# Kernel tuning notes

Measured on AMD Instinct MI355X. Metric: run time of the kernel, lower is better.

## Reference

```python
import jax, jax.numpy as jnp
import numpy as np

C = 1024
RANK = 8


def _layernorm(x, g, b, eps=1e-5):
    mu = jnp.mean(x, axis=-1, keepdims=True)
    var = jnp.var(x, axis=-1, keepdims=True)
    return (x - mu) * jax.lax.rsqrt(var + eps) * g + b


def setup_inputs() -> dict:
    key = jax.random.key(0)
    ks = jax.random.split(key, 10)
    B, T = 4, 4096
    x = jax.random.normal(ks[0], (B, T, C), dtype=jnp.float32)
    # parameters (match torch inits)
    W0 = jnp.eye(C, dtype=jnp.float32) * 0.1
    A_init = jax.random.normal(ks[1], (C, RANK), dtype=jnp.float32) * 0.01
    B_init = jnp.zeros((RANK, C), dtype=jnp.float32)
    log_lr = jnp.full((C,), float(np.log(0.1)), dtype=jnp.float32)
    s = 1.0 / np.sqrt(C)
    Wq = jax.random.uniform(ks[2], (C, C), minval=-s, maxval=s, dtype=jnp.float32)
    Wk = jax.random.uniform(ks[3], (C, C), minval=-s, maxval=s, dtype=jnp.float32)
    Wv = jax.random.uniform(ks[4], (C, C), minval=-s, maxval=s, dtype=jnp.float32)
    Wo = jax.random.uniform(ks[5], (C, C), minval=-s, maxval=s, dtype=jnp.float32)
    Wg = jax.random.uniform(ks[6], (C, C), minval=-s, maxval=s, dtype=jnp.float32)
    ln_g = jnp.ones((C,), dtype=jnp.float32)
    ln_b = jnp.zeros((C,), dtype=jnp.float32)
    ls_g = jnp.full((C,), 1e-4, dtype=jnp.float32)  # LayerScale gamma
    return {"x": x, "W0": W0, "A_init": A_init, "B_init": B_init,
            "log_lr": log_lr, "Wq": Wq, "Wk": Wk, "Wv": Wv, "Wo": Wo,
            "Wg": Wg, "ln_g": ln_g, "ln_b": ln_b, "ls_g": ls_g}


def reference(x, W0, A_init, B_init, log_lr, Wq, Wk, Wv, Wo, Wg, ln_g, ln_b, ls_g):
    B, T, _ = x.shape
    h = _layernorm(x, ln_g, ln_b)
    # dual-form TTT (training path: q/k/v projections, full K @ W0)
    Q = jnp.einsum('btc,dc->btd', h, Wq)
    K = jnp.einsum('btc,dc->btd', h, Wk)
    V = jnp.einsum('btc,dc->btd', h, Wv)
    lr = jnp.minimum(jnp.exp(log_lr), 1.0)  # clamp(max=1.0)
    y0 = jnp.einsum('btc,cd->btd', K, W0) + jnp.einsum('btr,rd->btd', jnp.einsum('btc,cr->btr', K, A_init), B_init)
    error = y0 - V
    loss = jnp.mean(error ** 2)
    gradient = K * error                     # [B,T,C]
    grad_cumsum = jnp.cumsum(gradient, axis=1)
    grad_shift = jnp.concatenate([jnp.zeros((B, 1, gradient.shape[-1]), gradient.dtype), grad_cumsum[:, :-1, :]], axis=1)
    correction = Q * lr[None, None, :] * grad_shift
    pos = jnp.arange(1, T + 1, dtype=correction.dtype)
    pos_scale = (1.0 / (1.0 + 0.1 * jnp.log(pos)))[None, :, None]
    out = y0 - correction * pos_scale
    # gate, out projection, layer scale, residual
    gate = jax.nn.sigmoid(jnp.einsum('btc,dc->btd', x, Wg))
    out = out * gate
    out = jnp.einsum('btc,dc->btd', out, Wo) * ls_g
    return (x + out, loss)
```

## Files before the change

### kernel.cpp

```cpp
#include <hip/hip_runtime.h>
#include <stdint.h>
#include <math.h>

typedef unsigned short u16;
typedef __attribute__((ext_vector_type(8))) short short8;
typedef __attribute__((ext_vector_type(4))) float f32x4;

__device__ __forceinline__ float bf2f(u16 u){
  union { unsigned int i; float f; } v; v.i = ((unsigned int)u) << 16; return v.f;
}
__device__ __forceinline__ u16 f2bf(float f){
  union { float f; unsigned int i; } v; v.f = f;
  return (u16)((v.i + 0x7FFFu + ((v.i >> 16) & 1u)) >> 16);
}

__global__ void ln_prep(const float* __restrict__ x, const float* __restrict__ g,
                        const float* __restrict__ bta, u16* __restrict__ h,
                        u16* __restrict__ xb, float* __restrict__ loss){
  if (blockIdx.x == 0 && threadIdx.x == 0) loss[0] = 0.f;
  int row = blockIdx.x, tid = threadIdx.x;
  const float4* xr = (const float4*)(x + (size_t)row * 1024);
  float4 v = xr[tid];
  float s  = v.x + v.y + v.z + v.w;
  float s2 = v.x*v.x + v.y*v.y + v.z*v.z + v.w*v.w;
  #pragma unroll
  for (int o = 32; o > 0; o >>= 1){ s += __shfl_down(s, o); s2 += __shfl_down(s2, o); }
  __shared__ float red[8];
  if ((tid & 63) == 0){ red[tid >> 6] = s; red[4 + (tid >> 6)] = s2; }
  __syncthreads();
  float ts = red[0]+red[1]+red[2]+red[3];
  float t2 = red[4]+red[5]+red[6]+red[7];
  float mu   = ts * (1.0f/1024.0f);
  float var  = t2 * (1.0f/1024.0f) - mu*mu;
  float rstd = rsqrtf(var + 1e-5f);
  float4 gg = ((const float4*)g)[tid];
  float4 bb = ((const float4*)bta)[tid];
  ushort4 hv, xv;
  hv.x = f2bf((v.x-mu)*rstd*gg.x + bb.x);
  hv.y = f2bf((v.y-mu)*rstd*gg.y + bb.y);
  hv.z = f2bf((v.z-mu)*rstd*gg.z + bb.z);
  hv.w = f2bf((v.w-mu)*rstd*gg.w + bb.w);
  xv.x = f2bf(v.x); xv.y = f2bf(v.y); xv.z = f2bf(v.z); xv.w = f2bf(v.w);
  ((ushort4*)h )[(size_t)row*256 + tid] = hv;
  ((ushort4*)xb)[(size_t)row*256 + tid] = xv;
}

__global__ void conv5(const float* __restrict__ a, const float* __restrict__ b,
                      const float* __restrict__ c, const float* __restrict__ d,
                      const float* __restrict__ e,
                      u16* oa, u16* ob, u16* oc, u16* od, u16* oe){
  int sel = blockIdx.y;
  const float* s = sel==0?a : sel==1?b : sel==2?c : sel==3?d : e;
  u16* o = sel==0?oa : sel==1?ob : sel==2?oc : sel==3?od : oe;
  int i = blockIdx.x*256 + threadIdx.x;
  float4 v = ((const float4*)s)[i];
  ushort4 r; r.x=f2bf(v.x); r.y=f2bf(v.y); r.z=f2bf(v.z); r.w=f2bf(v.w);
  ((ushort4*)o)[i] = r;
}

__global__ void weff_k(const float* __restrict__ W0, const float* __restrict__ Ai,
                       const float* __restrict__ Bi, u16* __restrict__ Wet){
  __shared__ float tile[32][33];
  int d0 = blockIdx.x*32, e0 = blockIdx.y*32;
  int tid = threadIdx.x;
  int lr = tid >> 5, lc = tid & 31;
  #pragma unroll
  for (int s = 0; s < 4; ++s){
    int e = e0 + s*8 + lr, d = d0 + lc;
    float v = W0[(size_t)e*1024 + d];
    #pragma unroll
    for (int r = 0; r < 8; ++r) v += Ai[e*8 + r] * Bi[(size_t)r*1024 + d];
    tile[s*8 + lr][lc] = v;
  }
  __syncthreads();
  #pragma unroll
  for (int s = 0; s < 4; ++s){
    int d = d0 + s*8 + lr, e = e0 + lc;
    Wet[(size_t)d*1024 + e] = f2bf(tile[lc][s*8 + lr]);
  }
}

#define VMW(N)  asm volatile("s_waitcnt vmcnt(" #N ")" ::: "memory")
#define SBAR    __builtin_amdgcn_s_barrier()
#define SCHED0  __builtin_amdgcn_sched_barrier(0)

template<int EPI>
__device__ __forceinline__ void gemm256_body(const u16* __restrict__ A, const u16* __restrict__ Bm,
    u16* __restrict__ Cb, float* __restrict__ Cf, const float* __restrict__ lsg,
    const float* __restrict__ xres, int mblk, int nblk)
{
  __shared__ u16 As[4][8192];
  __shared__ u16 Bs[4][8192];
  const int tid  = threadIdx.x;
  const int lane = tid & 63;
  const int w    = tid >> 6;
  const int wm = w >> 2, wn = w & 3;
  const int l15 = lane & 15, quad = lane >> 4;
  const int m0 = mblk * 256, n0 = nblk * 256;

  const int sl   = (lane & 7) ^ (lane >> 3);
  const int srow = 2*(w*8 + (lane >> 3)) + (sl >> 2);
  const int scol = (sl & 3) * 8;
  const u16* gA = A  + (size_t)(m0 + srow)*1024 + scol;
  const u16* gB = Bm + (size_t)(n0 + srow)*1024 + scol;
  const int ldsOff = w * 512;

  const int phys8 = (((((l15 & 1) << 2) | quad) ^ (l15 >> 1))) * 8;
  const int rdA = (wm*64 + (l15 >> 1))*64 + phys8;
  const int rdB = (wn*32 + (l15 >> 1))*64 + phys8;

  f32x4 acc[8][4] = {};

#define SA(T) do{ const int _ss=(T)&3; const size_t _k=(size_t)(T)*32; \
    __builtin_amdgcn_global_load_lds((const __attribute__((address_space(1))) unsigned int*)(gA + _k), \
        (__attribute__((address_space(3))) unsigned int*)(&As[_ss][ldsOff]), 16, 0, 0); \
    __builtin_amdgcn_global_load_lds((const __attribute__((address_space(1))) unsigned int*)(gA + _k + 131072), \
        (__attribute__((address_space(3))) unsigned int*)(&As[_ss][ldsOff + 4096]), 16, 0, 0); \
  }while(0)
#define SB(T) do{ const int _ss=(T)&3; const size_t _k=(size_t)(T)*32; \
    __builtin_amdgcn_global_load_lds((const __attribute__((address_space(1))) unsigned int*)(gB + _k), \
        (__attribute__((address_space(3))) unsigned int*)(&Bs[_ss][ldsOff]), 16, 0, 0); \
    __builtin_amdgcn_global_load_lds((const __attribute__((address_space(1))) unsigned int*)(gB + _k + 131072), \
        (__attribute__((address_space(3))) unsigned int*)(&Bs[_ss][ldsOff + 4096]), 16, 0, 0); \
  }while(0)

#define SLICE(T, VMOP, DS) do{ \
    VMOP; \
    SCHED0; SBAR; SCHED0; \
    if (DS){ SA((T)+3); SB((T)+3); } \
    const int _s = (T) & 3; \
    const u16* _as = &As[_s][0]; \
    const u16* _bs = &Bs[_s][0]; \
    short8 afv[8], bfv[4]; \
    _Pragma("unroll") \
    for (int _j = 0; _j < 4; ++_j) bfv[_j] = *(const short8*)(_bs + rdB + _j*512); \
    _Pragma("unroll") \
    for (int _i = 0; _i < 8; ++_i) afv[_i] = *(const short8*)(_as + rdA + _i*512); \
    _Pragma("unroll") \
    for (int _i = 0; _i < 8; ++_i){ \
      _Pragma("unroll") \
      for (int _j = 0; _j < 4; ++_j) \
        acc[_i][_j] = __builtin_amdgcn_mfma_f32_16x16x32_bf16(afv[_i], bfv[_j], acc[_i][_j], 0, 0, 0); \
    } \
  }while(0)

  SA(0); SB(0); SA(1); SB(1); SA(2); SB(2);

  #pragma unroll 1
  for (int t = 0; t < 28; t += 4){
    SLICE(t+0, VMW(8), 1);
    SLICE(t+1, VMW(8), 1);
    SLICE(t+2, VMW(8), 1);
    SLICE(t+3, VMW(8), 1);
  }
  SLICE(28, VMW(8), 1);
  SLICE(29, VMW(8), 0);
  SLICE(30, VMW(4), 0);
  SLICE(31, VMW(0), 0);
#undef SLICE
#undef SA
#undef SB

  const int rbase = quad * 4;
  if (EPI == 0){
    #pragma unroll
    for (int i = 0; i < 8; ++i){
      int row = m0 + wm*128 + i*16 + rbase;
      #pragma unroll
      for (int j = 0; j < 4; ++j){
        int col = n0 + wn*64 + j*16 + l15;
        #pragma unroll
        for (int r = 0; r < 4; ++r)
          Cb[(size_t)(row + r)*1024 + col] = f2bf(acc[i][j][r]);
      }
    }
  } else {
    float lsv[4];
    #pragma unroll
    for (int j = 0; j < 4; ++j) lsv[j] = lsg[n0 + wn*64 + j*16 + l15];
    #pragma unroll
    for (int i = 0; i < 8; ++i){
      int row = m0 + wm*128 + i*16 + rbase;
      #pragma unroll
      for (int j = 0; j < 4; ++j){
        int col = n0 + wn*64 + j*16 + l15;
        #pragma unroll
        for (int r = 0; r < 4; ++r){
          size_t idx = (size_t)(row + r)*1024 + col;
          Cf[idx] = acc[i][j][r] * lsv[j] + xres[idx];
        }
      }
    }
  }
}

__global__ __launch_bounds__(512, 2) void gemm_qkvg(
    const u16* __restrict__ h, const u16* __restrict__ xb,
    const u16* __restrict__ Wqb, const u16* __restrict__ Wkb,
    const u16* __restrict__ Wvb, const u16* __restrict__ Wgb,
    u16* __restrict__ Qb, u16* __restrict__ Kb,
    u16* __restrict__ Vb, u16* __restrict__ Gb){
  int bid = blockIdx.x;
  int swz = (bid & 7) * 128 + (bid >> 3);
  int mblk = swz >> 4;
  int rem  = swz & 15;
  int sel  = rem >> 2, nblk = rem & 3;
  const u16* A  = (sel == 3) ? xb : h;
  const u16* Bm = sel==0?Wqb : sel==1?Wkb : sel==2?Wvb : Wgb;
  u16* Out      = sel==0?Qb  : sel==1?Kb  : sel==2?Vb  : Gb;
  gemm256_body<0>(A, Bm, Out, nullptr, nullptr, nullptr, mblk, nblk);
}

__global__ __launch_bounds__(512, 2) void gemm_plain(
    const u16* __restrict__ A, const u16* __restrict__ Bm, u16* __restrict__ C){
  int bid = blockIdx.x;
  int swz = (bid & 7) * 32 + (bid >> 3);
  gemm256_body<0>(A, Bm, C, nullptr, nullptr, nullptr, swz >> 2, swz & 3);
}

__global__ __launch_bounds__(512, 2) void gemm_final(
    const u16* __restrict__ A, const u16* __restrict__ Bm,
    float* __restrict__ C, const float* __restrict__ lsg,
    const float* __restrict__ xres){
  int bid = blockIdx.x;
  int swz = (bid & 7) * 32 + (bid >> 3);
  gemm256_body<1>(A, Bm, nullptr, C, lsg, xres, swz >> 2, swz & 3);
}

__global__ void scan1(const u16* __restrict__ Kb, const u16* __restrict__ Vb,
                      const u16* __restrict__ Yb, float* __restrict__ part,
                      float* __restrict__ loss){
  int tid = threadIdx.x;
  int c = blockIdx.x*256 + tid;
  int ch = blockIdx.y, b = blockIdx.z;
  size_t base = ((size_t)b*4096 + (size_t)ch*128)*1024 + c;
  float g = 0.f, ls = 0.f;
  #pragma unroll 8
  for (int t = 0; t < 128; ++t){
    size_t idx = base + (size_t)t*1024;
    float kv = bf2f(Kb[idx]), vv = bf2f(Vb[idx]), yv = bf2f(Yb[idx]);
    float e = yv - vv;
    g += kv*e; ls += e*e;
  }
  part[((size_t)(b*32 + ch))*1024 + c] = g;
  #pragma unroll
  for (int o = 32; o > 0; o >>= 1) ls += __shfl_down(ls, o);
  __shared__ float red[4];
  if ((tid & 63) == 0) red[tid >> 6] = ls;
  __syncthreads();
  if (tid == 0) atomicAdd(loss, red[0]+red[1]+red[2]+red[3]);
}

__global__ void scan2(const u16* __restrict__ Kb, const u16* __restrict__ Vb,
                      const u16* __restrict__ Yb, const u16* __restrict__ Qb,
                      const u16* __restrict__ Gb, const float* __restrict__ part,
                      const float* __restrict__ llr, u16* __restrict__ OutPre){
  int tid = threadIdx.x;
  int c = blockIdx.x*256 + tid;
  int ch = blockIdx.y, b = blockIdx.z;
  float run = 0.f;
  for (int j = 0; j < ch; ++j) run += part[((size_t)(b*32 + j))*1024 + c];
  float lrc = fminf(expf(llr[c]), 1.0f);
  size_t base = ((size_t)b*4096 + (size_t)ch*128)*1024 + c;
  #pragma unroll 4
  for (int t = 0; t < 128; ++t){
    size_t idx = base + (size_t)t*1024;
    float kv = bf2f(Kb[idx]), vv = bf2f(Vb[idx]), yv = bf2f(Yb[idx]);
    float qv = bf2f(Qb[idx]), gl = bf2f(Gb[idx]);
    float e = yv - vv;
    int tg = ch*128 + t + 1;
    float ps = 1.0f/(1.0f + 0.1f*logf((float)tg));
    float gate = 1.0f/(1.0f + expf(-gl));
    float o = (yv - qv*lrc*run*ps) * gate;
    OutPre[idx] = f2bf(o);
    run += kv*e;
  }
}

__global__ void finloss(const float* __restrict__ loss, float* __restrict__ o){
  o[0] = loss[0] * (1.0f/16777216.0f);
}

extern "C" void kernel_launch(void* const* d_in, const int* in_sizes, int n_in,
                              void* d_out, int out_size, void* d_ws, size_t ws_size,
                              hipStream_t stream){
  const float* x   = (const float*)d_in[0];
  const float* W0  = (const float*)d_in[1];
  const float* Ai  = (const float*)d_in[2];
  const float* Bi  = (const float*)d_in[3];
  const float* llr = (const float*)d_in[4];
  const float* Wq  = (const float*)d_in[5];
  const float* Wk  = (const float*)d_in[6];
  const float* Wv  = (const float*)d_in[7];
  const float* Wo  = (const float*)d_in[8];
  const float* Wg  = (const float*)d_in[9];
  const float* lng = (const float*)d_in[10];
  const float* lnb = (const float*)d_in[11];
  const float* lsg = (const float*)d_in[12];
  float* out = (float*)d_out;

  const size_t TOK = 16384, CC = 1024;
  char* p = (char*)d_ws;
  float* loss = (float*)p; p += 256;
  u16* h   = (u16*)p; p += TOK*CC*2;
  u16* xb  = (u16*)p; p += TOK*CC*2;
  u16* Qb  = (u16*)p; p += TOK*CC*2;
  u16* Kb  = (u16*)p; p += TOK*CC*2;
  u16* Vb  = (u16*)p; p += TOK*CC*2;
  u16* Gb  = (u16*)p; p += TOK*CC*2;
  u16* Wqb = (u16*)p; p += CC*CC*2;
  u16* Wkb = (u16*)p; p += CC*CC*2;
  u16* Wvb = (u16*)p; p += CC*CC*2;
  u16* Wgb = (u16*)p; p += CC*CC*2;
  u16* Wob = (u16*)p; p += CC*CC*2;
  u16* Wet = (u16*)p; p += CC*CC*2;
  float* part = (float*)p; p += (size_t)4*32*1024*4;

  ln_prep<<<16384, 256, 0, stream>>>(x, lng, lnb, h, xb, loss);
  conv5<<<dim3(1024, 5), 256, 0, stream>>>(Wq, Wk, Wv, Wg, Wo, Wqb, Wkb, Wvb, Wgb, Wob);
  weff_k<<<dim3(32, 32), 256, 0, stream>>>(W0, Ai, Bi, Wet);
  gemm_qkvg<<<1024, 512, 0, stream>>>(h, xb, Wqb, Wkb, Wvb, Wgb, Qb, Kb, Vb, Gb);
  gemm_plain<<<256, 512, 0, stream>>>(Kb, Wet, h);
  scan1<<<dim3(4, 32, 4), 256, 0, stream>>>(Kb, Vb, h, part, loss);
  scan2<<<dim3(4, 32, 4), 256, 0, stream>>>(Kb, Vb, h, Qb, Gb, part, llr, Qb);
  gemm_final<<<256, 512, 0, stream>>>(Qb, Wob, out, lsg, x);
  finloss<<<1, 1, 0, stream>>>(loss, out + 16777216);
}
```

Measured before the change: 430.7 us.

## Switch GEMMs to 128x256 tiles with 4 waves and 3-stage LDS pipeline

Shrinks the GEMM block tile from 256x256 with 8 waves to 128x256 with 4 waves, each wave computing 64x128. Prefetch depth drops from a 4-stage to a 3-stage LDS ring, and MFMA sections are wrapped in s_setprio. The grids double to 2048/512/512 blocks so the wave count and tail behaviour change. Smaller tiles cut LDS use per block and may improve occupancy or load balance, but they lower data reuse per block and add more global traffic for B.

Measured after the change: 464.9 us. 7.9% more time.

```diff
diff --git a/kernel.cpp b/kernel.cpp
--- a/kernel.cpp
+++ b/kernel.cpp
@@ -85,18 +85,18 @@
 #define SCHED0  __builtin_amdgcn_sched_barrier(0)
 
 template<int EPI>
-__device__ __forceinline__ void gemm256_body(const u16* __restrict__ A, const u16* __restrict__ Bm,
+__device__ __forceinline__ void gemm128x256_body(const u16* __restrict__ A, const u16* __restrict__ Bm,
     u16* __restrict__ Cb, float* __restrict__ Cf, const float* __restrict__ lsg,
     const float* __restrict__ xres, int mblk, int nblk)
 {
-  __shared__ u16 As[4][8192];
-  __shared__ u16 Bs[4][8192];
+  __shared__ u16 As[3][4096];
+  __shared__ u16 Bs[3][8192];
   const int tid  = threadIdx.x;
   const int lane = tid & 63;
   const int w    = tid >> 6;
-  const int wm = w >> 2, wn = w & 3;
+  const int wr = w >> 1, wc = w & 1;
   const int l15 = lane & 15, quad = lane >> 4;
-  const int m0 = mblk * 256, n0 = nblk * 256;
+  const int m0 = mblk * 128, n0 = nblk * 256;
 
   const int sl   = (lane & 7) ^ (lane >> 3);
   const int srow = 2*(w*8 + (lane >> 3)) + (sl >> 2);
@@ -106,56 +106,59 @@
   const int ldsOff = w * 512;
 
   const int phys8 = (((((l15 & 1) << 2) | quad) ^ (l15 >> 1))) * 8;
-  const int rdA = (wm*64 + (l15 >> 1))*64 + phys8;
-  const int rdB = (wn*32 + (l15 >> 1))*64 + phys8;
-
-  f32x4 acc[8][4] = {};
-
-#define SA(T) do{ const int _ss=(T)&3; const size_t _k=(size_t)(T)*32; \
+  const int rdA = (wr*32 + (l15 >> 1))*64 + phys8;
+  const int rdB = (wc*64 + (l15 >> 1))*64 + phys8;
+
+  f32x4 acc[4][8] = {};
+
+#define SA(T) do{ const int _ss=(T)%3; const size_t _k=(size_t)(T)*32; \
     __builtin_amdgcn_global_load_lds((const __attribute__((address_space(1))) unsigned int*)(gA + _k), \
         (__attribute__((address_space(3))) unsigned int*)(&As[_ss][ldsOff]), 16, 0, 0); \
-    __builtin_amdgcn_global_load_lds((const __attribute__((address_space(1))) unsigned int*)(gA + _k + 131072), \
-        (__attribute__((address_space(3))) unsigned int*)(&As[_ss][ldsOff + 4096]), 16, 0, 0); \
+    __builtin_amdgcn_global_load_lds((const __attribute__((address_space(1))) unsigned int*)(gA + _k + 65536), \
+        (__attribute__((address_space(3))) unsigned int*)(&As[_ss][ldsOff + 2048]), 16, 0, 0); \
   }while(0)
-#define SB(T) do{ const int _ss=(T)&3; const size_t _k=(size_t)(T)*32; \
+#define SB(T) do{ const int _ss=(T)%3; const size_t _k=(size_t)(T)*32; \
     __builtin_amdgcn_global_load_lds((const __attribute__((address_space(1))) unsigned int*)(gB + _k), \
         (__attribute__((address_space(3))) unsigned int*)(&Bs[_ss][ldsOff]), 16, 0, 0); \
+    __builtin_amdgcn_global_load_lds((const __attribute__((address_space(1))) unsigned int*)(gB + _k + 65536), \
+        (__attribute__((address_space(3))) unsigned int*)(&Bs[_ss][ldsOff + 2048]), 16, 0, 0); \
     __builtin_amdgcn_global_load_lds((const __attribute__((address_space(1))) unsigned int*)(gB + _k + 131072), \
         (__attribute__((address_space(3))) unsigned int*)(&Bs[_ss][ldsOff + 4096]), 16, 0, 0); \
+    __builtin_amdgcn_global_load_lds((const __attribute__((address_space(1))) unsigned int*)(gB + _k + 196608), \
+        (__attribute__((address_space(3))) unsigned int*)(&Bs[_ss][ldsOff + 6144]), 16, 0, 0); \
   }while(0)
 
 #define SLICE(T, VMOP, DS) do{ \
     VMOP; \
     SCHED0; SBAR; SCHED0; \
-    if (DS){ SA((T)+3); SB((T)+3); } \
-    const int _s = (T) & 3; \
+    if (DS){ SA((T)+2); SB((T)+2); } \
+    const int _s = (T) % 3; \
     const u16* _as = &As[_s][0]; \
     const u16* _bs = &Bs[_s][0]; \
-    short8 afv[8], bfv[4]; \
+    short8 afv[4], bfv[8]; \
     _Pragma("unroll") \
-    for (int _j = 0; _j < 4; ++_j) bfv[_j] = *(const short8*)(_bs + rdB + _j*512); \
+    for (int _i = 0; _i < 4; ++_i) afv[_i] = *(const short8*)(_as + rdA + _i*512); \
     _Pragma("unroll") \
-    for (int _i = 0; _i < 8; ++_i) afv[_i] = *(const short8*)(_as + rdA + _i*512); \
+    for (int _j = 0; _j < 8; ++_j) bfv[_j] = *(const short8*)(_bs + rdB + _j*512); \
+    __builtin_amdgcn_s_setprio(1); \
     _Pragma("unroll") \
-    for (int _i = 0; _i < 8; ++_i){ \
+    for (int _i = 0; _i < 4; ++_i){ \
       _Pragma("unroll") \
-      for (int _j = 0; _j < 4; ++_j) \
+      for (int _j = 0; _j < 8; ++_j) \
         acc[_i][_j] = __builtin_amdgcn_mfma_f32_16x16x32_bf16(afv[_i], bfv[_j], acc[_i][_j], 0, 0, 0); \
     } \
+    __builtin_amdgcn_s_setprio(0); \
   }while(0)
 
-  SA(0); SB(0); SA(1); SB(1); SA(2); SB(2);
+  SA(0); SB(0); SA(1); SB(1);
 
   #pragma unroll 1
-  for (int t = 0; t < 28; t += 4){
-    SLICE(t+0, VMW(8), 1);
-    SLICE(t+1, VMW(8), 1);
-    SLICE(t+2, VMW(8), 1);
-    SLICE(t+3, VMW(8), 1);
-  }
-  SLICE(28, VMW(8), 1);
-  SLICE(29, VMW(8), 0);
-  SLICE(30, VMW(4), 0);
+  for (int t = 0; t < 30; t += 3){
+    SLICE(t+0, VMW(6), 1);
+    SLICE(t+1, VMW(6), 1);
+    SLICE(t+2, VMW(6), 1);
+  }
+  SLICE(30, VMW(6), 0);
   SLICE(31, VMW(0), 0);
 #undef SLICE
 #undef SA
@@ -164,26 +167,26 @@
   const int rbase = quad * 4;
   if (EPI == 0){
     #pragma unroll
-    for (int i = 0; i < 8; ++i){
-      int row = m0 + wm*128 + i*16 + rbase;
+    for (int i = 0; i < 4; ++i){
+      int row = m0 + wr*64 + i*16 + rbase;
       #pragma unroll
-      for (int j = 0; j < 4; ++j){
-        int col = n0 + wn*64 + j*16 + l15;
+      for (int j = 0; j < 8; ++j){
+        int col = n0 + wc*128 + j*16 + l15;
         #pragma unroll
         for (int r = 0; r < 4; ++r)
           Cb[(size_t)(row + r)*1024 + col] = f2bf(acc[i][j][r]);
       }
     }
   } else {
-    float lsv[4];
+    float lsv[8];
     #pragma unroll
-    for (int j = 0; j < 4; ++j) lsv[j] = lsg[n0 + wn*64 + j*16 + l15];
+    for (int j = 0; j < 8; ++j) lsv[j] = lsg[n0 + wc*128 + j*16 + l15];
     #pragma unroll
-    for (int i = 0; i < 8; ++i){
-      int row = m0 + wm*128 + i*16 + rbase;
+    for (int i = 0; i < 4; ++i){
+      int row = m0 + wr*64 + i*16 + rbase;
       #pragma unroll
-      for (int j = 0; j < 4; ++j){
-        int col = n0 + wn*64 + j*16 + l15;
+      for (int j = 0; j < 8; ++j){
+        int col = n0 + wc*128 + j*16 + l15;
         #pragma unroll
         for (int r = 0; r < 4; ++r){
           size_t idx = (size_t)(row + r)*1024 + col;
@@ -194,37 +197,37 @@
   }
 }
 
-__global__ __launch_bounds__(512, 2) void gemm_qkvg(
+__global__ __launch_bounds__(256, 2) void gemm_qkvg(
     const u16* __restrict__ h, const u16* __restrict__ xb,
     const u16* __restrict__ Wqb, const u16* __restrict__ Wkb,
     const u16* __restrict__ Wvb, const u16* __restrict__ Wgb,
     u16* __restrict__ Qb, u16* __restrict__ Kb,
     u16* __restrict__ Vb, u16* __restrict__ Gb){
   int bid = blockIdx.x;
-  int swz = (bid & 7) * 128 + (bid >> 3);
+  int swz = (bid & 7) * 256 + (bid >> 3);
   int mblk = swz >> 4;
   int rem  = swz & 15;
   int sel  = rem >> 2, nblk = rem & 3;
   const u16* A  = (sel == 3) ? xb : h;
   const u16* Bm = sel==0?Wqb : sel==1?Wkb : sel==2?Wvb : Wgb;
   u16* Out      = sel==0?Qb  : sel==1?Kb  : sel==2?Vb  : Gb;
-  gemm256_body<0>(A, Bm, Out, nullptr, nullptr, nullptr, mblk, nblk);
-}
-
-__global__ __launch_bounds__(512, 2) void gemm_plain(
+  gemm128x256_body<0>(A, Bm, Out, nullptr, nullptr, nullptr, mblk, nblk);
+}
+
+__global__ __launch_bounds__(256, 2) void gemm_plain(
     const u16* __restrict__ A, const u16* __restrict__ Bm, u16* __restrict__ C){
   int bid = blockIdx.x;
-  int swz = (bid & 7) * 32 + (bid >> 3);
-  gemm256_body<0>(A, Bm, C, nullptr, nullptr, nullptr, swz >> 2, swz & 3);
-}
-
-__global__ __launch_bounds__(512, 2) void gemm_final(
+  int swz = (bid & 7) * 64 + (bid >> 3);
+  gemm128x256_body<0>(A, Bm, C, nullptr, nullptr, nullptr, swz >> 2, swz & 3);
+}
+
+__global__ __launch_bounds__(256, 2) void gemm_final(
     const u16* __restrict__ A, const u16* __restrict__ Bm,
     float* __restrict__ C, const float* __restrict__ lsg,
     const float* __restrict__ xres){
   int bid = blockIdx.x;
-  int swz = (bid & 7) * 32 + (bid >> 3);
-  gemm256_body<1>(A, Bm, nullptr, C, lsg, xres, swz >> 2, swz & 3);
+  int swz = (bid & 7) * 64 + (bid >> 3);
+  gemm128x256_body<1>(A, Bm, nullptr, C, lsg, xres, swz >> 2, swz & 3);
 }
 
 __global__ void scan1(const u16* __restrict__ Kb, const u16* __restrict__ Vb,
@@ -319,10 +322,10 @@
   ln_prep<<<16384, 256, 0, stream>>>(x, lng, lnb, h, xb, loss);
   conv5<<<dim3(1024, 5), 256, 0, stream>>>(Wq, Wk, Wv, Wg, Wo, Wqb, Wkb, Wvb, Wgb, Wob);
   weff_k<<<dim3(32, 32), 256, 0, stream>>>(W0, Ai, Bi, Wet);
-  gemm_qkvg<<<1024, 512, 0, stream>>>(h, xb, Wqb, Wkb, Wvb, Wgb, Qb, Kb, Vb, Gb);
-  gemm_plain<<<256, 512, 0, stream>>>(Kb, Wet, h);
+  gemm_qkvg<<<2048, 256, 0, stream>>>(h, xb, Wqb, Wkb, Wvb, Wgb, Qb, Kb, Vb, Gb);
+  gemm_plain<<<512, 256, 0, stream>>>(Kb, Wet, h);
   scan1<<<dim3(4, 32, 4), 256, 0, stream>>>(Kb, Vb, h, part, loss);
   scan2<<<dim3(4, 32, 4), 256, 0, stream>>>(Kb, Vb, h, Qb, Gb, part, llr, Qb);
-  gemm_final<<<256, 512, 0, stream>>>(Qb, Wob, out, lsg, x);
+  gemm_final<<<512, 256, 0, stream>>>(Qb, Wob, out, lsg, x);
   finloss<<<1, 1, 0, stream>>>(loss, out + 16777216);
 }
```

## Fuse the first scan pass into the y0 GEMM epilogue

Applied to the files above, without the earlier changes.

Replaces the separate scan1 kernel with an epilogue on the K·Weff GEMM. The epilogue computes the error against V, the per-chunk gradient partial sums over 128-row chunks via cross-quad shuffles, and the loss via wave reductions and atomics. This removes one kernel launch and one full re-read of the K, V and Y0 buffers. In exchange the epilogue does extra scattered bf16 loads of V and K per element, and issues many more atomic loss adds (one per wave).

Result: slower. 462.5 us (+7.4%).

```diff
diff --git a/kernel.cpp b/kernel.cpp
--- a/kernel.cpp
+++ b/kernel.cpp
@@ -87,7 +87,8 @@
 template<int EPI>
 __device__ __forceinline__ void gemm256_body(const u16* __restrict__ A, const u16* __restrict__ Bm,
     u16* __restrict__ Cb, float* __restrict__ Cf, const float* __restrict__ lsg,
-    const float* __restrict__ xres, int mblk, int nblk)
+    const float* __restrict__ xres, const u16* __restrict__ Vv,
+    float* __restrict__ part, float* __restrict__ loss, int mblk, int nblk)
 {
   __shared__ u16 As[4][8192];
   __shared__ u16 Bs[4][8192];
@@ -174,7 +175,7 @@
           Cb[(size_t)(row + r)*1024 + col] = f2bf(acc[i][j][r]);
       }
     }
-  } else {
+  } else if (EPI == 1){
     float lsv[4];
     #pragma unroll
     for (int j = 0; j < 4; ++j) lsv[j] = lsg[n0 + wn*64 + j*16 + l15];
@@ -191,6 +192,41 @@
         }
       }
     }
+  } else {
+    float g0=0.f, g1=0.f, g2=0.f, g3=0.f, ls=0.f;
+    #pragma unroll
+    for (int i = 0; i < 8; ++i){
+      int row = m0 + wm*128 + i*16 + rbase;
+      #pragma unroll
+      for (int j = 0; j < 4; ++j){
+        int col = n0 + wn*64 + j*16 + l15;
+        #pragma unroll
+        for (int r = 0; r < 4; ++r){
+          size_t idx = (size_t)(row + r)*1024 + col;
+          u16 yb = f2bf(acc[i][j][r]);
+          Cb[idx] = yb;
+          float e = bf2f(yb) - bf2f(Vv[idx]);
+          float kv = bf2f(A[idx]);
+          ls += e*e;
+          float ge = kv*e;
+          if (j == 0) g0 += ge; else if (j == 1) g1 += ge;
+          else if (j == 2) g2 += ge; else g3 += ge;
+        }
+      }
+    }
+    g0 += __shfl_xor(g0, 16); g0 += __shfl_xor(g0, 32);
+    g1 += __shfl_xor(g1, 16); g1 += __shfl_xor(g1, 32);
+    g2 += __shfl_xor(g2, 16); g2 += __shfl_xor(g2, 32);
+    g3 += __shfl_xor(g3, 16); g3 += __shfl_xor(g3, 32);
+    float gw = (quad == 0) ? g0 : (quad == 1) ? g1 : (quad == 2) ? g2 : g3;
+    int rowc = m0 + wm*128;
+    int bb   = rowc >> 12;
+    int ch   = (rowc & 4095) >> 7;
+    int colq = n0 + wn*64 + quad*16 + l15;
+    part[((size_t)(bb*32 + ch))*1024 + colq] = gw;
+    #pragma unroll
+    for (int o = 32; o > 0; o >>= 1) ls += __shfl_down(ls, o);
+    if (lane == 0) atomicAdd(loss, ls);
   }
 }
 
@@ -208,14 +244,16 @@
   const u16* A  = (sel == 3) ? xb : h;
   const u16* Bm = sel==0?Wqb : sel==1?Wkb : sel==2?Wvb : Wgb;
   u16* Out      = sel==0?Qb  : sel==1?Kb  : sel==2?Vb  : Gb;
-  gemm256_body<0>(A, Bm, Out, nullptr, nullptr, nullptr, mblk, nblk);
-}
-
-__global__ __launch_bounds__(512, 2) void gemm_plain(
-    const u16* __restrict__ A, const u16* __restrict__ Bm, u16* __restrict__ C){
+  gemm256_body<0>(A, Bm, Out, nullptr, nullptr, nullptr, nullptr, nullptr, nullptr, mblk, nblk);
+}
+
+__global__ __launch_bounds__(512, 2) void gemm_y0scan(
+    const u16* __restrict__ Kb, const u16* __restrict__ Wet,
+    u16* __restrict__ Y0, const u16* __restrict__ Vb,
+    float* __restrict__ part, float* __restrict__ loss){
   int bid = blockIdx.x;
   int swz = (bid & 7) * 32 + (bid >> 3);
-  gemm256_body<0>(A, Bm, C, nullptr, nullptr, nullptr, swz >> 2, swz & 3);
+  gemm256_body<2>(Kb, Wet, Y0, nullptr, nullptr, nullptr, Vb, part, loss, swz >> 2, swz & 3);
 }
 
 __global__ __launch_bounds__(512, 2) void gemm_final(
@@ -224,31 +262,7 @@
     const float* __restrict__ xres){
   int bid = blockIdx.x;
   int swz = (bid & 7) * 32 + (bid >> 3);
-  gemm256_body<1>(A, Bm, nullptr, C, lsg, xres, swz >> 2, swz & 3);
-}
-
-__global__ void scan1(const u16* __restrict__ Kb, const u16* __restrict__ Vb,
-                      const u16* __restrict__ Yb, float* __restrict__ part,
-                      float* __restrict__ loss){
-  int tid = threadIdx.x;
-  int c = blockIdx.x*256 + tid;
-  int ch = blockIdx.y, b = blockIdx.z;
-  size_t base = ((size_t)b*4096 + (size_t)ch*128)*1024 + c;
-  float g = 0.f, ls = 0.f;
-  #pragma unroll 8
-  for (int t = 0; t < 128; ++t){
-    size_t idx = base + (size_t)t*1024;
-    float kv = bf2f(Kb[idx]), vv = bf2f(Vb[idx]), yv = bf2f(Yb[idx]);
-    float e = yv - vv;
-    g += kv*e; ls += e*e;
-  }
-  part[((size_t)(b*32 + ch))*1024 + c] = g;
-  #pragma unroll
-  for (int o = 32; o > 0; o >>= 1) ls += __shfl_down(ls, o);
-  __shared__ float red[4];
-  if ((tid & 63) == 0) red[tid >> 6] = ls;
-  __syncthreads();
-  if (tid == 0) atomicAdd(loss, red[0]+red[1]+red[2]+red[3]);
+  gemm256_body<1>(A, Bm, nullptr, C, lsg, xres, nullptr, nullptr, nullptr, swz >> 2, swz & 3);
 }
 
 __global__ void scan2(const u16* __restrict__ Kb, const u16* __restrict__ Vb,
@@ -320,8 +334,7 @@
   conv5<<<dim3(1024, 5), 256, 0, stream>>>(Wq, Wk, Wv, Wg, Wo, Wqb, Wkb, Wvb, Wgb, Wob);
   weff_k<<<dim3(32, 32), 256, 0, stream>>>(W0, Ai, Bi, Wet);
   gemm_qkvg<<<1024, 512, 0, stream>>>(h, xb, Wqb, Wkb, Wvb, Wgb, Qb, Kb, Vb, Gb);
-  gemm_plain<<<256, 512, 0, stream>>>(Kb, Wet, h);
-  scan1<<<dim3(4, 32, 4), 256, 0, stream>>>(Kb, Vb, h, part, loss);
+  gemm_y0scan<<<256, 512, 0, stream>>>(Kb, Wet, h, Vb, part, loss);
   scan2<<<dim3(4, 32, 4), 256, 0, stream>>>(Kb, Vb, h, Qb, Gb, part, llr, Qb);
   gemm_final<<<256, 512, 0, stream>>>(Qb, Wob, out, lsg, x);
   finloss<<<1, 1, 0, stream>>>(loss, out + 16777216);
```
